# Performance work log

Hardware: AMD Instinct MI355X
Metric: run time of the kernel (lower is better)

## Reference

```python
import jax, jax.numpy as jnp
import numpy as np

N_TOKENS = 16384
MODEL_DIM = 2048
NUM_EXPERTS = 64
K = 2


def setup_inputs() -> dict:
    key = jax.random.key(0)
    k1, k2 = jax.random.split(key)
    inputs = jax.random.normal(k1, (N_TOKENS, MODEL_DIM), dtype=jnp.float32)
    # gate weight, torch Linear(model_dim, num_experts, bias=False) -> [E, D]
    wg_weight = jax.random.normal(k2, (NUM_EXPERTS, MODEL_DIM), dtype=jnp.float32) * 0.02
    return {"inputs": inputs, "wg_weight": wg_weight}


def reference(inputs, wg_weight):
    E = wg_weight.shape[0]
    # gate computed in fp32 (module casts input and keeps wg in float32)
    logits = jnp.einsum("nd,ed->ne", inputs.astype(jnp.float32), wg_weight)
    probs = jax.nn.softmax(logits, axis=-1)                      # [N, E]
    topk_probs, topk_indices = jax.lax.top_k(probs, K)           # [N, K]
    flat_idx = topk_indices.reshape(-1)                          # [N*K]
    # stable sort of expert ids over all (token, slot) pairs
    sort_ordering = jnp.argsort(flat_idx)                        # [N*K]
    # reverse permutation: reversed[sort_ordering[i]] = i
    ar = jnp.arange(flat_idx.shape[0], dtype=sort_ordering.dtype)
    reversed_ordering = jnp.zeros_like(sort_ordering).at[sort_ordering].set(ar)
    # map slot index back to token index
    token_order = sort_ordering // K
    # per-expert counts (== unique_consecutive counts scattered into [E])
    input_splits = jnp.bincount(flat_idx, length=E).astype(jnp.int64)
    # combine weights: renormalize top-k probs via softmax when k > 1
    if K > 1:
        combine_weights = jax.nn.softmax(topk_probs, axis=-1)
    else:
        combine_weights = topk_probs
    combine_weights = combine_weights.reshape(-1).astype(inputs.dtype)
    return token_order, reversed_ordering, combine_weights, input_splits, probs
```

## Files before the change

### kernel.cpp

```cpp
#include <hip/hip_runtime.h>
#include <math.h>

#define N_TOKENS    16384
#define MODEL_DIM   2048
#define NUM_EXPERTS 64
#define NK          (N_TOKENS * 2)

#define OFF_TOKEN_ORDER 0
#define OFF_REVERSED    (NK)
#define OFF_COMBINE     (2 * NK)
#define OFF_SPLITS      (3 * NK)
#define OFF_PROBS       (3 * NK + NUM_EXPERTS)

#define NSEG 256
#define NFRAG 16384

typedef _Float16 half8 __attribute__((ext_vector_type(8)));
typedef float    f32x4 __attribute__((ext_vector_type(4)));

#define IMIN(a, b) ((a) < (b) ? (a) : (b))

__global__ __launch_bounds__(256) void preconvert(
    const float* __restrict__ w, half8* __restrict__ WH, half8* __restrict__ WL,
    int* __restrict__ segHist)
{
    const int fr = blockIdx.x * 256 + threadIdx.x;
    const int lane = fr & 63;
    const int tile = (fr >> 6) & 3;
    const int kstep = fr >> 8;
    const int e = tile * 16 + (lane & 15);
    const int kb = kstep * 32 + (lane >> 4) * 8;
    const float* src = w + (size_t)e * MODEL_DIM + kb;
    const float4 w0 = *(const float4*)(src);
    const float4 w1 = *(const float4*)(src + 4);
    const float av[8] = {w0.x, w0.y, w0.z, w0.w, w1.x, w1.y, w1.z, w1.w};
    half8 hh, hl;
#pragma unroll
    for (int j = 0; j < 8; j++) {
        const float v = av[j] * 64.0f;
        const _Float16 h = (_Float16)v;
        hh[j] = h;
        hl[j] = (_Float16)((v - (float)h) * 4096.0f);
    }
    WH[fr] = hh;
    WL[fr] = hl;
    segHist[fr] = 0;
}


#define LOADB(BH_, BL_, G_) do {                                            \
    const size_t bb_ = (size_t)(G_) * 256 + lane;                           \
    _Pragma("unroll")                                                       \
    for (int t_ = 0; t_ < 4; t_++) {                                        \
        BH_[t_] = WH[bb_ + t_ * 64];                                        \
        BL_[t_] = WL[bb_ + t_ * 64];                                        \
    }                                                                       \
} while (0)

#define LOADA(DST_, KOFF_) do {                                             \
    const int ko_ = (KOFF_);                                                \
    _Pragma("unroll")                                                       \
    for (int s_ = 0; s_ < 4; s_++) {                                        \
        DST_[2*s_]   = *(const float4*)(px + ko_ + s_*32);                  \
        DST_[2*s_+1] = *(const float4*)(px + ko_ + s_*32 + 4);              \
    }                                                                       \
} while (0)

#define STEP(AV_, SI_, BHC_, BLC_, BHN_, BLN_, GN_) do {                    \
    LOADB(BHN_, BLN_, GN_);                                                 \
    const float4 A0_ = AV_[2*(SI_)];                                        \
    const float4 A1_ = AV_[2*(SI_)+1];                                      \
    const float av_[8] = {A0_.x,A0_.y,A0_.z,A0_.w,A1_.x,A1_.y,A1_.z,A1_.w}; \
    half8 ah_, al_;                                                         \
    _Pragma("unroll")                                                       \
    for (int j_ = 0; j_ < 8; j_++) {                                        \
        const float v_ = av_[j_];                                           \
        const _Float16 h_ = (_Float16)v_;                                   \
        ah_[j_] = h_;                                                       \
        al_[j_] = (_Float16)((v_ - (float)h_) * 4096.0f);                   \
    }                                                                       \
    _Pragma("unroll")                                                       \
    for (int t_ = 0; t_ < 4; t_++) {                                        \
        accH[t_] = __builtin_amdgcn_mfma_f32_16x16x32_f16(ah_, BHC_[t_], accH[t_], 0, 0, 0); \
        accC[t_] = __builtin_amdgcn_mfma_f32_16x16x32_f16(ah_, BLC_[t_], accC[t_], 0, 0, 0); \
        accC[t_] = __builtin_amdgcn_mfma_f32_16x16x32_f16(al_, BHC_[t_], accC[t_], 0, 0, 0); \
    }                                                                       \
} while (0)

__global__ __launch_bounds__(128, 2) void gate_fused(
    const float* __restrict__ x, const half8* __restrict__ WH,
    const half8* __restrict__ WL, float* __restrict__ out,
    int* __restrict__ flat_idx, int* __restrict__ segHist)
{
    __shared__ double lds_d[64 * 17];

    const int tid = threadIdx.x;
    const int wv = tid >> 6;
    const int lane = tid & 63;
    const int t0 = blockIdx.x * 16;
    const int col = lane & 15;
    const int kg = lane >> 4;

    const float* px = x + (size_t)(t0 + col) * MODEL_DIM + wv * 1024 + kg * 8;
    const int gbase = wv * 32;

    f32x4 accH[4], accC[4];
    double accD[4][4];
#pragma unroll
    for (int t = 0; t < 4; t++) {
        accH[t] = (f32x4){0.f, 0.f, 0.f, 0.f};
        accC[t] = (f32x4){0.f, 0.f, 0.f, 0.f};
#pragma unroll
        for (int r = 0; r < 4; r++) accD[t][r] = 0.0;
    }

    float4 aA[8], aB[8];
    half8 bh0[4], bl0[4], bh1[4], bl1[4];

    LOADA(aA, 0);
    LOADB(bh0, bl0, gbase);

    for (int it = 0; it < 4; it++) {
        const int ss = it * 2;
        const int gb = gbase + it * 8;
        LOADA(aB, (ss + 1) * 128);
        STEP(aA, 0, bh0, bl0, bh1, bl1, IMIN(gb + 1, 63));
        STEP(aA, 1, bh1, bl1, bh0, bl0, IMIN(gb + 2, 63));
        STEP(aA, 2, bh0, bl0, bh1, bl1, IMIN(gb + 3, 63));
        STEP(aA, 3, bh1, bl1, bh0, bl0, IMIN(gb + 4, 63));
        LOADA(aA, IMIN(ss + 2, 7) * 128);
        STEP(aB, 0, bh0, bl0, bh1, bl1, IMIN(gb + 5, 63));
        STEP(aB, 1, bh1, bl1, bh0, bl0, IMIN(gb + 6, 63));
        STEP(aB, 2, bh0, bl0, bh1, bl1, IMIN(gb + 7, 63));
        STEP(aB, 3, bh1, bl1, bh0, bl0, IMIN(gb + 8, 63));
#pragma unroll
        for (int t = 0; t < 4; t++)
#pragma unroll
            for (int r = 0; r < 4; r++) {
                accD[t][r] += (double)accH[t][r] + (double)accC[t][r] * (1.0 / 4096.0);
                accH[t][r] = 0.0f;
                accC[t][r] = 0.0f;
            }
    }

    if (wv == 1) {
#pragma unroll
        for (int t = 0; t < 4; t++)
#pragma unroll
            for (int r = 0; r < 4; r++)
                lds_d[lane * 17 + t * 4 + r] = accD[t][r];
    }
    __syncthreads();
    if (wv == 1) return;

#pragma unroll
    for (int t = 0; t < 4; t++)
#pragma unroll
        for (int r = 0; r < 4; r++)
            accD[t][r] += lds_d[lane * 17 + t * 4 + r];

    const int rowg = lane >> 4;
#pragma unroll
    for (int r = 0; r < 4; r++) {
        float lv[4];
#pragma unroll
        for (int t = 0; t < 4; t++) lv[t] = (float)(accD[t][r] * (1.0 / 64.0));

        float m = fmaxf(fmaxf(lv[0], lv[1]), fmaxf(lv[2], lv[3]));
#pragma unroll
        for (int d = 1; d < 16; d <<= 1) m = fmaxf(m, __shfl_xor(m, d));

        float l1 = -INFINITY, l2 = -INFINITY;
        int i1 = 0, i2 = 0;
#pragma unroll
        for (int t = 0; t < 4; t++) {
            const float l = lv[t];
            const int e = t * 16 + col;
            if (l > l1)      { l2 = l1; i2 = i1; l1 = l; i1 = e; }
            else if (l > l2) { l2 = l;  i2 = e; }
        }
#pragma unroll
        for (int d = 1; d < 16; d <<= 1) {
            const float ol1 = __shfl_xor(l1, d), ol2 = __shfl_xor(l2, d);
            const int   oi1 = __shfl_xor(i1, d), oi2 = __shfl_xor(i2, d);
            if (ol1 > l1 || (ol1 == l1 && oi1 < i1)) {
                if (l1 > ol2 || (l1 == ol2 && i1 < oi2)) { l2 = l1;  i2 = i1;  }
                else                                     { l2 = ol2; i2 = oi2; }
                l1 = ol1; i1 = oi1;
            } else if (ol1 > l2 || (ol1 == l2 && oi1 < i2)) {
                l2 = ol1; i2 = oi1;
            }
        }

        float ex[4];
        double sd = 0.0;
#pragma unroll
        for (int t = 0; t < 4; t++) { ex[t] = expf(lv[t] - m); sd += (double)ex[t]; }
#pragma unroll
        for (int d = 1; d < 16; d <<= 1) sd += __shfl_xor(sd, d);
        const float inv = (float)(1.0 / sd);

        const int tok = t0 + rowg * 4 + r;
        float* pp = out + OFF_PROBS + (size_t)tok * NUM_EXPERTS + col;
#pragma unroll
        for (int t = 0; t < 4; t++) pp[t * 16] = ex[t] * inv;

        if (col == 0) {
            const float p1 = expf(l1 - m) * inv;
            const float p2 = expf(l2 - m) * inv;
            const float e2 = expf(p2 - p1);
            const float rr = 1.0f / (1.0f + e2);
            out[OFF_COMBINE + 2 * tok]     = rr;
            out[OFF_COMBINE + 2 * tok + 1] = e2 * rr;
            flat_idx[2 * tok]     = i1;
            flat_idx[2 * tok + 1] = i2;
            atomicAdd(&segHist[(tok >> 6) * NUM_EXPERTS + i1], 1);
            atomicAdd(&segHist[(tok >> 6) * NUM_EXPERTS + i2], 1);
        }
    }
}

__global__ __launch_bounds__(256) void scan_kernel(
    const int* __restrict__ segHist, int* __restrict__ segOff,
    float* __restrict__ out)
{
    __shared__ int h[NSEG * NUM_EXPERTS];
    __shared__ int gtot[4 * NUM_EXPERTS];
    __shared__ int base[NUM_EXPERTS];
    const int tid = threadIdx.x;
    for (int i = tid; i < NSEG * NUM_EXPERTS / 4; i += 256)
        *(int4*)(h + i * 4) = *(const int4*)(segHist + i * 4);
    __syncthreads();

    const int e = tid & 63;
    const int g = tid >> 6;
    int run = 0;
    for (int s = g * 64; s < g * 64 + 64; s++) {
        const int idx = s * NUM_EXPERTS + e;
        const int v = h[idx];
        h[idx] = run;
        run += v;
    }
    gtot[g * NUM_EXPERTS + e] = run;
    __syncthreads();

    if (tid < NUM_EXPERTS) {
        int b = 0;
#pragma unroll
        for (int gg = 0; gg < 4; gg++) {
            const int t = gtot[gg * NUM_EXPERTS + tid];
            gtot[gg * NUM_EXPERTS + tid] = b;
            b += t;
        }
        out[OFF_SPLITS + tid] = (float)b;
        int xs = b;
#pragma unroll
        for (int off = 1; off < 64; off <<= 1) {
            const int v = __shfl_up(xs, off);
            if (tid >= off) xs += v;
        }
        base[tid] = xs - b;
    }
    __syncthreads();

    const int myoff = gtot[g * NUM_EXPERTS + e] + base[e];
    for (int s = g * 64; s < g * 64 + 64; s++) {
        const int idx = s * NUM_EXPERTS + e;
        segOff[idx] = h[idx] + myoff;
    }
}

__global__ __launch_bounds__(256) void scatter_kernel(
    const int* __restrict__ flat_idx, const int* __restrict__ segOff,
    float* __restrict__ out)
{
    __shared__ int cnt[2 * NUM_EXPERTS];
    const int tid = threadIdx.x;
    const int i = blockIdx.x * 256 + tid;
    const int e = flat_idx[i];
    const int lane = tid & 63;
    const int wv = tid >> 6;
    const int segslot = wv >> 1;
    const int seg = i >> 7;

    if (tid < 2 * NUM_EXPERTS) cnt[tid] = 0;
    __syncthreads();

    unsigned long long match = ~0ull;
#pragma unroll
    for (int b = 0; b < 6; b++) {
        const unsigned long long m = __ballot((e >> b) & 1);
        match &= ((e >> b) & 1) ? m : ~m;
    }
    const int rank = __popcll(match & ((1ull << lane) - 1ull));

    int pos = 0;
    if ((wv & 1) == 0) {
        pos = segOff[seg * NUM_EXPERTS + e] + rank;
        if (lane == __builtin_ctzll(match))
            cnt[segslot * NUM_EXPERTS + e] = __popcll(match);
    }
    __syncthreads();
    if ((wv & 1) == 1)
        pos = segOff[seg * NUM_EXPERTS + e] + cnt[segslot * NUM_EXPERTS + e] + rank;

    out[OFF_TOKEN_ORDER + pos] = (float)(i >> 1);
    out[OFF_REVERSED + i]      = (float)pos;
}

extern "C" void kernel_launch(void* const* d_in, const int* in_sizes, int n_in,
                              void* d_out, int out_size, void* d_ws, size_t ws_size,
                              hipStream_t stream) {
    const float* x = (const float*)d_in[0];
    const float* w = (const float*)d_in[1];
    float* out = (float*)d_out;

    int* flat_idx = (int*)d_ws;
    int* segHist  = flat_idx + NK;
    int* segOff   = segHist + NSEG * NUM_EXPERTS;
    half8* WH = (half8*)(segOff + NSEG * NUM_EXPERTS);
    half8* WL = WH + NFRAG;

    preconvert<<<64, 256, 0, stream>>>(w, WH, WL, segHist);
    gate_fused<<<N_TOKENS / 16, 128, 0, stream>>>(x, WH, WL, out, flat_idx, segHist);
    scan_kernel<<<1, 256, 0, stream>>>(segHist, segOff, out);
    scatter_kernel<<<NK / 256, 256, 0, stream>>>(flat_idx, segOff, out);
}
```

Measured before the change: 245.2 us.

## Stage gate GEMM operands through LDS with async double-buffered global_load_lds

The gate GEMM kernel now stages both the weight fragments and the input rows into double-buffered shared memory using direct global-to-LDS loads, instead of loading them into registers per wave. Each block grows to four waves covering 32 tokens, so every weight fragment fetched is shared by two token groups. The aim is to halve weight traffic per token and overlap the next stage's loads with the current MFMA work. In exchange it adds two barriers per k-step, plus LDS pressure that may limit occupancy.

```diff
diff --git a/kernel.cpp b/kernel.cpp
--- a/kernel.cpp
+++ b/kernel.cpp
@@ -15,10 +15,20 @@
 #define NSEG 256
 #define NFRAG 16384
 
+#define B_BYTES  16384
+#define A_BYTES  8192
+#define STAGE_BYTES (B_BYTES + A_BYTES)
+
 typedef _Float16 half8 __attribute__((ext_vector_type(8)));
 typedef float    f32x4 __attribute__((ext_vector_type(4)));
 
-#define IMIN(a, b) ((a) < (b) ? (a) : (b))
+#define MEMFENCE asm volatile("" ::: "memory")
+
+__device__ __forceinline__ void glds16(const void* g, void* l) {
+    __builtin_amdgcn_global_load_lds(
+        (const __attribute__((address_space(1))) void*)g,
+        (__attribute__((address_space(3))) void*)l, 16, 0, 0);
+}
 
 __global__ __launch_bounds__(256) void preconvert(
     const float* __restrict__ w, half8* __restrict__ WH, half8* __restrict__ WL,
@@ -47,62 +57,48 @@
     segHist[fr] = 0;
 }
 
-
-#define LOADB(BH_, BL_, G_) do {                                            \
-    const size_t bb_ = (size_t)(G_) * 256 + lane;                           \
-    _Pragma("unroll")                                                       \
-    for (int t_ = 0; t_ < 4; t_++) {                                        \
-        BH_[t_] = WH[bb_ + t_ * 64];                                        \
-        BL_[t_] = WL[bb_ + t_ * 64];                                        \
-    }                                                                       \
-} while (0)
-
-#define LOADA(DST_, KOFF_) do {                                             \
-    const int ko_ = (KOFF_);                                                \
-    _Pragma("unroll")                                                       \
-    for (int s_ = 0; s_ < 4; s_++) {                                        \
-        DST_[2*s_]   = *(const float4*)(px + ko_ + s_*32);                  \
-        DST_[2*s_+1] = *(const float4*)(px + ko_ + s_*32 + 4);              \
-    }                                                                       \
-} while (0)
-
-#define STEP(AV_, SI_, BHC_, BLC_, BHN_, BLN_, GN_) do {                    \
-    LOADB(BHN_, BLN_, GN_);                                                 \
-    const float4 A0_ = AV_[2*(SI_)];                                        \
-    const float4 A1_ = AV_[2*(SI_)+1];                                      \
-    const float av_[8] = {A0_.x,A0_.y,A0_.z,A0_.w,A1_.x,A1_.y,A1_.z,A1_.w}; \
-    half8 ah_, al_;                                                         \
-    _Pragma("unroll")                                                       \
-    for (int j_ = 0; j_ < 8; j_++) {                                        \
-        const float v_ = av_[j_];                                           \
-        const _Float16 h_ = (_Float16)v_;                                   \
-        ah_[j_] = h_;                                                       \
-        al_[j_] = (_Float16)((v_ - (float)h_) * 4096.0f);                   \
-    }                                                                       \
-    _Pragma("unroll")                                                       \
-    for (int t_ = 0; t_ < 4; t_++) {                                        \
-        accH[t_] = __builtin_amdgcn_mfma_f32_16x16x32_f16(ah_, BHC_[t_], accH[t_], 0, 0, 0); \
-        accC[t_] = __builtin_amdgcn_mfma_f32_16x16x32_f16(ah_, BLC_[t_], accC[t_], 0, 0, 0); \
-        accC[t_] = __builtin_amdgcn_mfma_f32_16x16x32_f16(al_, BHC_[t_], accC[t_], 0, 0, 0); \
-    }                                                                       \
-} while (0)
-
-__global__ __launch_bounds__(128, 2) void gate_fused(
+__global__ __launch_bounds__(256, 2) void gate_fused(
     const float* __restrict__ x, const half8* __restrict__ WH,
     const half8* __restrict__ WL, float* __restrict__ out,
     int* __restrict__ flat_idx, int* __restrict__ segHist)
 {
-    __shared__ double lds_d[64 * 17];
-
-    const int tid = threadIdx.x;
-    const int wv = tid >> 6;
+    __shared__ alignas(16) unsigned char smem[2 * STAGE_BYTES];
+
+    const int tid  = threadIdx.x;
+    const int wv   = tid >> 6;
     const int lane = tid & 63;
-    const int t0 = blockIdx.x * 16;
-    const int col = lane & 15;
-    const int kg = lane >> 4;
-
-    const float* px = x + (size_t)(t0 + col) * MODEL_DIM + wv * 1024 + kg * 8;
-    const int gbase = wv * 32;
+    const int kh   = wv & 1;
+    const int tg   = wv >> 1;
+    const int t0   = blockIdx.x * 32;
+    const int col  = lane & 15;
+    const int kg   = lane >> 4;
+
+    const unsigned char* s_ptr[6];
+    int s_stride[6];
+    int s_off[6];
+#pragma unroll
+    for (int i = 0; i < 6; i++) {
+        const int c = wv * 6 + i;
+        if (c < 16) {
+            const int hl   = c & 1;
+            const int tile = (c >> 1) & 3;
+            const int ckh  = c >> 3;
+            const half8* base = (hl ? WL : WH) + ((size_t)((ckh * 32) * 4 + tile) * 64 + lane);
+            s_ptr[i]    = (const unsigned char*)base;
+            s_stride[i] = 4096;
+            s_off[i]    = c * 1024 + lane * 16;
+        } else {
+            const int a   = c - 16;
+            const int cc  = a & 1;
+            const int ctg = (a >> 1) & 1;
+            const int ckh = a >> 2;
+            const float* base = x + (size_t)(t0 + ctg * 16 + (lane & 15)) * MODEL_DIM
+                              + ckh * 1024 + (lane >> 4) * 8 + cc * 4;
+            s_ptr[i]    = (const unsigned char*)base;
+            s_stride[i] = 128;
+            s_off[i]    = B_BYTES + a * 1024 + lane * 16;
+        }
+    }
 
     f32x4 accH[4], accC[4];
     double accD[4][4];
@@ -114,50 +110,80 @@
         for (int r = 0; r < 4; r++) accD[t][r] = 0.0;
     }
 
-    float4 aA[8], aB[8];
-    half8 bh0[4], bl0[4], bh1[4], bl1[4];
-
-    LOADA(aA, 0);
-    LOADB(bh0, bl0, gbase);
-
-    for (int it = 0; it < 4; it++) {
-        const int ss = it * 2;
-        const int gb = gbase + it * 8;
-        LOADA(aB, (ss + 1) * 128);
-        STEP(aA, 0, bh0, bl0, bh1, bl1, IMIN(gb + 1, 63));
-        STEP(aA, 1, bh1, bl1, bh0, bl0, IMIN(gb + 2, 63));
-        STEP(aA, 2, bh0, bl0, bh1, bl1, IMIN(gb + 3, 63));
-        STEP(aA, 3, bh1, bl1, bh0, bl0, IMIN(gb + 4, 63));
-        LOADA(aA, IMIN(ss + 2, 7) * 128);
-        STEP(aB, 0, bh0, bl0, bh1, bl1, IMIN(gb + 5, 63));
-        STEP(aB, 1, bh1, bl1, bh0, bl0, IMIN(gb + 6, 63));
-        STEP(aB, 2, bh0, bl0, bh1, bl1, IMIN(gb + 7, 63));
-        STEP(aB, 3, bh1, bl1, bh0, bl0, IMIN(gb + 8, 63));
+#pragma unroll
+    for (int i = 0; i < 6; i++) glds16(s_ptr[i], smem + s_off[i]);
+
+    const int aoff = B_BYTES + (kh * 4 + tg * 2) * 1024 + lane * 16;
+    const int boff = (kh * 4) * 2048 + lane * 16;
+
+    for (int j = 0; j < 32; j++) {
+        const int jn = (j < 31) ? j + 1 : 31;
+        unsigned char* nbuf = smem + ((j + 1) & 1) * STAGE_BYTES;
+#pragma unroll
+        for (int i = 0; i < 6; i++)
+            glds16(s_ptr[i] + (size_t)jn * s_stride[i], nbuf + s_off[i]);
+
+        asm volatile("s_waitcnt vmcnt(6)" ::: "memory");
+        __builtin_amdgcn_s_barrier();
+        MEMFENCE;
+
+        const unsigned char* buf = smem + (j & 1) * STAGE_BYTES;
+
+        const float4 a0 = *(const float4*)(buf + aoff);
+        const float4 a1 = *(const float4*)(buf + aoff + 1024);
+        const float av[8] = {a0.x, a0.y, a0.z, a0.w, a1.x, a1.y, a1.z, a1.w};
+        half8 ah, al;
+#pragma unroll
+        for (int q = 0; q < 8; q++) {
+            const float v = av[q];
+            const _Float16 h = (_Float16)v;
+            ah[q] = h;
+            al[q] = (_Float16)((v - (float)h) * 4096.0f);
+        }
+
+#pragma unroll
+        for (int t = 0; t < 4; t++) {
+            const half8 bh = *(const half8*)(buf + boff + t * 2048);
+            const half8 bl = *(const half8*)(buf + boff + t * 2048 + 1024);
+            accH[t] = __builtin_amdgcn_mfma_f32_16x16x32_f16(ah, bh, accH[t], 0, 0, 0);
+            accC[t] = __builtin_amdgcn_mfma_f32_16x16x32_f16(ah, bl, accC[t], 0, 0, 0);
+            accC[t] = __builtin_amdgcn_mfma_f32_16x16x32_f16(al, bh, accC[t], 0, 0, 0);
+        }
+
+        if ((j & 7) == 7) {
+#pragma unroll
+            for (int t = 0; t < 4; t++)
+#pragma unroll
+                for (int r = 0; r < 4; r++) {
+                    accD[t][r] += (double)accH[t][r] + (double)accC[t][r] * (1.0 / 4096.0);
+                    accH[t][r] = 0.0f;
+                    accC[t][r] = 0.0f;
+                }
+        }
+
+        MEMFENCE;
+        __builtin_amdgcn_s_barrier();
+    }
+
+    asm volatile("s_waitcnt vmcnt(0)" ::: "memory");
+    __syncthreads();
+
+    double* red = (double*)smem;
+    if (kh == 1) {
 #pragma unroll
         for (int t = 0; t < 4; t++)
 #pragma unroll
-            for (int r = 0; r < 4; r++) {
-                accD[t][r] += (double)accH[t][r] + (double)accC[t][r] * (1.0 / 4096.0);
-                accH[t][r] = 0.0f;
-                accC[t][r] = 0.0f;
-            }
-    }
-
-    if (wv == 1) {
-#pragma unroll
-        for (int t = 0; t < 4; t++)
-#pragma unroll
             for (int r = 0; r < 4; r++)
-                lds_d[lane * 17 + t * 4 + r] = accD[t][r];
-    }
-    __syncthreads();
-    if (wv == 1) return;
+                red[(tg * 64 + lane) * 17 + t * 4 + r] = accD[t][r];
+    }
+    __syncthreads();
+    if (kh == 1) return;
 
 #pragma unroll
     for (int t = 0; t < 4; t++)
 #pragma unroll
         for (int r = 0; r < 4; r++)
-            accD[t][r] += lds_d[lane * 17 + t * 4 + r];
+            accD[t][r] += red[(tg * 64 + lane) * 17 + t * 4 + r];
 
     const int rowg = lane >> 4;
 #pragma unroll
@@ -200,7 +226,7 @@
         for (int d = 1; d < 16; d <<= 1) sd += __shfl_xor(sd, d);
         const float inv = (float)(1.0 / sd);
 
-        const int tok = t0 + rowg * 4 + r;
+        const int tok = t0 + tg * 16 + rowg * 4 + r;
         float* pp = out + OFF_PROBS + (size_t)tok * NUM_EXPERTS + col;
 #pragma unroll
         for (int t = 0; t < 4; t++) pp[t * 16] = ex[t] * inv;
@@ -322,7 +348,7 @@
     half8* WL = WH + NFRAG;
 
     preconvert<<<64, 256, 0, stream>>>(w, WH, WL, segHist);
-    gate_fused<<<N_TOKENS / 16, 128, 0, stream>>>(x, WH, WL, out, flat_idx, segHist);
+    gate_fused<<<512, 256, 0, stream>>>(x, WH, WL, out, flat_idx, segHist);
     scan_kernel<<<1, 256, 0, stream>>>(segHist, segOff, out);
     scatter_kernel<<<NK / 256, 256, 0, stream>>>(flat_idx, segOff, out);
 }
```

Measured after the change: 224.8 us. 1.09x faster.
